# Performance work log

Measured on AMD Instinct MI355X. Metric: run time of the kernel, lower is better.

The kernel has to match this reference:

```python
import jax, jax.numpy as jnp
import numpy as np

B, S, D = 32, 4096, 256

def setup_inputs() -> dict:
    key = jax.random.key(0)
    k1, k2, k3 = jax.random.split(key, 3)
    inputs = jax.random.normal(k1, (B, S, D), dtype=jnp.float32)
    W = jax.random.normal(k2, (D, D), dtype=jnp.float32) * 0.05  # 'random_normal' init
    b = jnp.zeros((D,), dtype=jnp.float32)
    V = jax.random.normal(k3, (D, 1), dtype=jnp.float32) * 0.05
    return {"inputs": inputs, "W": W, "b": b, "V": V}

def reference(inputs, W, b, V):
    # score: [B,S,D] = tanh(inputs @ W + b)
    score = jnp.tanh(jnp.einsum('bsd,de->bse', inputs, W) + b)
    # logits: [B,S,1]; softmax over seq axis (axis=1)
    logits = jnp.einsum('bsd,do->bso', score, V)
    attn = jax.nn.softmax(logits, axis=1)            # [B,S,1]
    # weighted sum pooling over seq -> [B,D]
    context = jnp.sum(attn * inputs, axis=1)
    return context
```

## Files before the change

kernel.cpp:

```cpp
#include <hip/hip_runtime.h>
#include <hip/hip_bf16.h>

#define DD 256
#define SS 4096

typedef __bf16 bf16x8 __attribute__((ext_vector_type(8)));
typedef float  f32x4  __attribute__((ext_vector_type(4)));

__device__ __forceinline__ float fast_tanh(float x) {
  float e = __expf(2.0f * x);
  return 1.0f - 2.0f / (e + 1.0f);
}

template<int CTRL>
__device__ __forceinline__ float dpp_mov(float v) {
  return __int_as_float(__builtin_amdgcn_update_dpp(0, __float_as_int(v), CTRL, 0xF, 0xF, true));
}
__device__ __forceinline__ float row16_sum(float v) {
  v += dpp_mov<0xB1>(v);
  v += dpp_mov<0x4E>(v);
  v += dpp_mov<0x124>(v);
  v += dpp_mov<0x128>(v);
  return v;
}
__device__ __forceinline__ float row16_max(float v) {
  v = fmaxf(v, dpp_mov<0xB1>(v));
  v = fmaxf(v, dpp_mov<0x4E>(v));
  v = fmaxf(v, dpp_mov<0x124>(v));
  v = fmaxf(v, dpp_mov<0x128>(v));
  return v;
}

__global__ __launch_bounds__(1024, 1) __attribute__((amdgpu_waves_per_eu(4)))
void fused_kernel(
    const float* __restrict__ X, const float* __restrict__ W,
    const float* __restrict__ bias, const float* __restrict__ V,
    float* __restrict__ Pout, float* __restrict__ Mout, float* __restrict__ Sout)
{
  __shared__ __bf16 WtF[8192 * 8];
  __shared__ float  Pacc[16][DD];
  __shared__ float  Vs[DD];
  __shared__ float  Bs[DD];
  __shared__ float  wred[16];
  __shared__ float  sred[16];

  const int t = threadIdx.x;
  for (int c = t; c < 8192; c += 1024) {
    const int lane_c = c & 63;
    const int ks  = (c >> 6) & 7;
    const int n0  = c >> 9;
    const int col = n0 * 16 + (lane_c & 15);
    const int k0  = ks * 32 + (lane_c >> 4) * 8;
    const float* wp = W + k0 * DD + col;
    bf16x8 fr;
    #pragma unroll
    for (int i = 0; i < 8; ++i) fr[i] = (__bf16)wp[i * DD];
    *reinterpret_cast<bf16x8*>(&WtF[(size_t)c * 8]) = fr;
  }
  if (t < DD) { Vs[t] = V[t]; Bs[t] = bias[t]; }
  __syncthreads();

  const int wave = t >> 6, lane = t & 63;
  const int g  = lane >> 4;
  const int lg = lane & 15;
  const size_t rowBase = (size_t)blockIdx.x * 512 + (size_t)wave * 32;

  bf16x8 a[2][8];
  #pragma unroll
  for (int st = 0; st < 2; ++st) {
    const float* xr = X + (rowBase + st * 16 + lg) * DD;
    #pragma unroll
    for (int ks = 0; ks < 8; ++ks) {
      const float4* p = reinterpret_cast<const float4*>(xr + ks * 32 + g * 8);
      float4 f0 = p[0], f1 = p[1];
      bf16x8 fr;
      fr[0] = (__bf16)f0.x; fr[1] = (__bf16)f0.y; fr[2] = (__bf16)f0.z; fr[3] = (__bf16)f0.w;
      fr[4] = (__bf16)f1.x; fr[5] = (__bf16)f1.y; fr[6] = (__bf16)f1.z; fr[7] = (__bf16)f1.w;
      a[st][ks] = fr;
    }
  }

  float sp0[4] = {0.f,0.f,0.f,0.f};
  float sp1[4] = {0.f,0.f,0.f,0.f};
  #pragma unroll 1
  for (int n0 = 0; n0 < 16; ++n0) {
    const __bf16* bp = WtF + ((size_t)(n0 * 8) * 64 + lane) * 8;
    f32x4 acc0 = {0.f,0.f,0.f,0.f};
    f32x4 acc1 = {0.f,0.f,0.f,0.f};
    #pragma unroll
    for (int ks = 0; ks < 8; ++ks) {
      bf16x8 bfr = *reinterpret_cast<const bf16x8*>(bp + (size_t)ks * 64 * 8);
      acc0 = __builtin_amdgcn_mfma_f32_16x16x32_bf16(a[0][ks], bfr, acc0, 0, 0, 0);
      acc1 = __builtin_amdgcn_mfma_f32_16x16x32_bf16(a[1][ks], bfr, acc1, 0, 0, 0);
    }
    const int col = n0 * 16 + lg;
    const float vc = Vs[col], bc = Bs[col];
    #pragma unroll
    for (int r = 0; r < 4; ++r) {
      sp0[r] += fast_tanh(acc0[r] + bc) * vc;
      sp1[r] += fast_tanh(acc1[r] + bc) * vc;
    }
  }

  #pragma unroll
  for (int r = 0; r < 4; ++r) { sp0[r] = row16_sum(sp0[r]); sp1[r] = row16_sum(sp1[r]); }

  const int src = ((lg >> 2) << 4) | lg;
  float l0 = 0.f, l1 = 0.f;
  #pragma unroll
  for (int r = 0; r < 4; ++r) {
    float v0 = __shfl(sp0[r], src, 64);
    float v1 = __shfl(sp1[r], src, 64);
    if ((lg & 3) == r) { l0 = v0; l1 = v1; }
  }

  float wm = row16_max(fmaxf(l0, l1));
  if (lane == 0) wred[wave] = wm;
  __syncthreads();
  float M = -1e30f;
  #pragma unroll
  for (int w = 0; w < 16; ++w) M = fmaxf(M, wred[w]);

  const float w0 = __expf(l0 - M);
  const float w1 = __expf(l1 - M);

  float se = row16_sum(w0 + w1);
  if (lane == 0) sred[wave] = se;

  #pragma unroll
  for (int ks = 0; ks < 8; ++ks) {
    float p8[8];
    #pragma unroll
    for (int i = 0; i < 8; ++i)
      p8[i] = w0 * (float)a[0][ks][i] + w1 * (float)a[1][ks][i];
    #pragma unroll
    for (int i = 0; i < 8; ++i) p8[i] = row16_sum(p8[i]);
    if (lg < 2) {
      float4 v = (lg == 0) ? make_float4(p8[0], p8[1], p8[2], p8[3])
                           : make_float4(p8[4], p8[5], p8[6], p8[7]);
      *reinterpret_cast<float4*>(&Pacc[wave][ks * 32 + g * 8 + lg * 4]) = v;
    }
  }
  __syncthreads();

  if (t < DD) {
    float s = 0.f;
    #pragma unroll
    for (int w = 0; w < 16; ++w) s += Pacc[w][t];
    Pout[(size_t)blockIdx.x * DD + t] = s;
  }
  if (t == 0) {
    float ss = 0.f;
    #pragma unroll
    for (int w = 0; w < 16; ++w) ss += sred[w];
    Sout[blockIdx.x] = ss;
    Mout[blockIdx.x] = M;
  }
}

__global__ __launch_bounds__(256) void combine_kernel(
    const float* __restrict__ P, const float* __restrict__ Mb,
    const float* __restrict__ Sb, float* __restrict__ ctx)
{
  const int b = blockIdx.x, t = threadIdx.x;
  float Mg = -1e30f;
  #pragma unroll
  for (int k = 0; k < 8; ++k) Mg = fmaxf(Mg, Mb[b * 8 + k]);
  float denom = 0.f, acc = 0.f;
  #pragma unroll
  for (int k = 0; k < 8; ++k) {
    const float f = __expf(Mb[b * 8 + k] - Mg);
    denom += f * Sb[b * 8 + k];
    acc   += f * P[(size_t)(b * 8 + k) * DD + t];
  }
  ctx[b * DD + t] = acc / denom;
}

extern "C" void kernel_launch(void* const* d_in, const int* in_sizes, int n_in,
                              void* d_out, int out_size, void* d_ws, size_t ws_size,
                              hipStream_t stream) {
  const float* X    = (const float*)d_in[0];
  const float* W    = (const float*)d_in[1];
  const float* bias = (const float*)d_in[2];
  const float* V    = (const float*)d_in[3];
  float* ctx = (float*)d_out;

  float* P = (float*)d_ws;
  float* M = P + 256 * DD;
  float* S = M + 256;

  fused_kernel<<<256, 1024, 0, stream>>>(X, W, bias, V, P, M, S);
  combine_kernel<<<32, 256, 0, stream>>>(P, M, S, ctx);
}
```

Baseline: 51.45 us.

## Pre-swizzle W to bf16 in global memory and stream B-fragments with double buffering

W is now converted and swizzled to bf16 fragments once by a separate prep kernel into workspace, instead of every block rebuilding a 128KB LDS copy. The fused kernel reads B fragments straight from global/L2 with a two-buffer register prefetch, and uses 512 blocks of 512 threads, so more blocks fit per CU and more waves are resident. This removes the per-block W staging cost and the large LDS footprint, at the cost of an extra launch, repeated L2 reads of W, more register pressure, and a combine over 16 partials per batch.

```diff
diff --git a/kernel.cpp b/kernel.cpp
--- a/kernel.cpp
+++ b/kernel.cpp
@@ -31,39 +31,61 @@
   return v;
 }
 
-__global__ __launch_bounds__(1024, 1) __attribute__((amdgpu_waves_per_eu(4)))
-void fused_kernel(
-    const float* __restrict__ X, const float* __restrict__ W,
+__global__ __launch_bounds__(256) void prep_kernel(
+    const float* __restrict__ W, __bf16* __restrict__ WF)
+{
+  const int c = blockIdx.x * 256 + threadIdx.x;
+  const int lane_c = c & 63;
+  const int ks  = (c >> 6) & 7;
+  const int n0  = c >> 9;
+  const int col = n0 * 16 + (lane_c & 15);
+  const int k0  = ks * 32 + (lane_c >> 4) * 8;
+  const float* wp = W + k0 * DD + col;
+  bf16x8 fr;
+  #pragma unroll
+  for (int i = 0; i < 8; ++i) fr[i] = (__bf16)wp[i * DD];
+  *reinterpret_cast<bf16x8*>(WF + (size_t)c * 8) = fr;
+}
+
+#define LOADB(buf, n0q) { \
+  const bf16x8* _src = WFv + ((n0q) * 8 * 64 + lane); \
+  _Pragma("unroll") \
+  for (int _ks = 0; _ks < 8; ++_ks) buf[_ks] = _src[_ks * 64]; }
+
+#define COMPUTE(buf, n0q) { \
+  f32x4 _acc0 = {0.f,0.f,0.f,0.f}; \
+  f32x4 _acc1 = {0.f,0.f,0.f,0.f}; \
+  _Pragma("unroll") \
+  for (int _ks = 0; _ks < 8; ++_ks) { \
+    _acc0 = __builtin_amdgcn_mfma_f32_16x16x32_bf16(a[0][_ks], buf[_ks], _acc0, 0, 0, 0); \
+    _acc1 = __builtin_amdgcn_mfma_f32_16x16x32_bf16(a[1][_ks], buf[_ks], _acc1, 0, 0, 0); } \
+  const int _col = (n0q) * 16 + lg; \
+  const float _vc = Vs[_col], _bc = Bs[_col]; \
+  _Pragma("unroll") \
+  for (int _r = 0; _r < 4; ++_r) { \
+    sp0[_r] += fast_tanh(_acc0[_r] + _bc) * _vc; \
+    sp1[_r] += fast_tanh(_acc1[_r] + _bc) * _vc; } }
+
+__global__ __launch_bounds__(512, 4) void fused_kernel(
+    const float* __restrict__ X, const __bf16* __restrict__ WF,
     const float* __restrict__ bias, const float* __restrict__ V,
     float* __restrict__ Pout, float* __restrict__ Mout, float* __restrict__ Sout)
 {
-  __shared__ __bf16 WtF[8192 * 8];
-  __shared__ float  Pacc[16][DD];
-  __shared__ float  Vs[DD];
-  __shared__ float  Bs[DD];
-  __shared__ float  wred[16];
-  __shared__ float  sred[16];
+  __shared__ float Pacc[8][DD];
+  __shared__ float Vs[DD];
+  __shared__ float Bs[DD];
+  __shared__ float wred[8];
+  __shared__ float sred[8];
 
   const int t = threadIdx.x;
-  for (int c = t; c < 8192; c += 1024) {
-    const int lane_c = c & 63;
-    const int ks  = (c >> 6) & 7;
-    const int n0  = c >> 9;
-    const int col = n0 * 16 + (lane_c & 15);
-    const int k0  = ks * 32 + (lane_c >> 4) * 8;
-    const float* wp = W + k0 * DD + col;
-    bf16x8 fr;
-    #pragma unroll
-    for (int i = 0; i < 8; ++i) fr[i] = (__bf16)wp[i * DD];
-    *reinterpret_cast<bf16x8*>(&WtF[(size_t)c * 8]) = fr;
-  }
   if (t < DD) { Vs[t] = V[t]; Bs[t] = bias[t]; }
   __syncthreads();
 
   const int wave = t >> 6, lane = t & 63;
   const int g  = lane >> 4;
   const int lg = lane & 15;
-  const size_t rowBase = (size_t)blockIdx.x * 512 + (size_t)wave * 32;
+  const size_t rowBase = (size_t)blockIdx.x * 256 + (size_t)wave * 32;
+  const bf16x8* WFv = reinterpret_cast<const bf16x8*>(WF);
 
   bf16x8 a[2][8];
   #pragma unroll
@@ -82,24 +104,14 @@
 
   float sp0[4] = {0.f,0.f,0.f,0.f};
   float sp1[4] = {0.f,0.f,0.f,0.f};
-  #pragma unroll 1
-  for (int n0 = 0; n0 < 16; ++n0) {
-    const __bf16* bp = WtF + ((size_t)(n0 * 8) * 64 + lane) * 8;
-    f32x4 acc0 = {0.f,0.f,0.f,0.f};
-    f32x4 acc1 = {0.f,0.f,0.f,0.f};
-    #pragma unroll
-    for (int ks = 0; ks < 8; ++ks) {
-      bf16x8 bfr = *reinterpret_cast<const bf16x8*>(bp + (size_t)ks * 64 * 8);
-      acc0 = __builtin_amdgcn_mfma_f32_16x16x32_bf16(a[0][ks], bfr, acc0, 0, 0, 0);
-      acc1 = __builtin_amdgcn_mfma_f32_16x16x32_bf16(a[1][ks], bfr, acc1, 0, 0, 0);
-    }
-    const int col = n0 * 16 + lg;
-    const float vc = Vs[col], bc = Bs[col];
-    #pragma unroll
-    for (int r = 0; r < 4; ++r) {
-      sp0[r] += fast_tanh(acc0[r] + bc) * vc;
-      sp1[r] += fast_tanh(acc1[r] + bc) * vc;
-    }
+  bf16x8 bufA[8], bufB[8];
+  LOADB(bufA, 0);
+  #pragma unroll
+  for (int n2 = 0; n2 < 8; ++n2) {
+    LOADB(bufB, n2 * 2 + 1);
+    COMPUTE(bufA, n2 * 2);
+    if (n2 < 7) LOADB(bufA, n2 * 2 + 2);
+    COMPUTE(bufB, n2 * 2 + 1);
   }
 
   #pragma unroll
@@ -119,7 +131,7 @@
   __syncthreads();
   float M = -1e30f;
   #pragma unroll
-  for (int w = 0; w < 16; ++w) M = fmaxf(M, wred[w]);
+  for (int w = 0; w < 8; ++w) M = fmaxf(M, wred[w]);
 
   const float w0 = __expf(l0 - M);
   const float w1 = __expf(l1 - M);
@@ -146,13 +158,13 @@
   if (t < DD) {
     float s = 0.f;
     #pragma unroll
-    for (int w = 0; w < 16; ++w) s += Pacc[w][t];
+    for (int w = 0; w < 8; ++w) s += Pacc[w][t];
     Pout[(size_t)blockIdx.x * DD + t] = s;
   }
   if (t == 0) {
     float ss = 0.f;
     #pragma unroll
-    for (int w = 0; w < 16; ++w) ss += sred[w];
+    for (int w = 0; w < 8; ++w) ss += sred[w];
     Sout[blockIdx.x] = ss;
     Mout[blockIdx.x] = M;
   }
@@ -165,13 +177,13 @@
   const int b = blockIdx.x, t = threadIdx.x;
   float Mg = -1e30f;
   #pragma unroll
-  for (int k = 0; k < 8; ++k) Mg = fmaxf(Mg, Mb[b * 8 + k]);
+  for (int k = 0; k < 16; ++k) Mg = fmaxf(Mg, Mb[b * 16 + k]);
   float denom = 0.f, acc = 0.f;
   #pragma unroll
-  for (int k = 0; k < 8; ++k) {
-    const float f = __expf(Mb[b * 8 + k] - Mg);
-    denom += f * Sb[b * 8 + k];
-    acc   += f * P[(size_t)(b * 8 + k) * DD + t];
+  for (int k = 0; k < 16; ++k) {
+    const float f = __expf(Mb[b * 16 + k] - Mg);
+    denom += f * Sb[b * 16 + k];
+    acc   += f * P[(size_t)(b * 16 + k) * DD + t];
   }
   ctx[b * DD + t] = acc / denom;
 }
@@ -185,10 +197,12 @@
   const float* V    = (const float*)d_in[3];
   float* ctx = (float*)d_out;
 
-  float* P = (float*)d_ws;
-  float* M = P + 256 * DD;
-  float* S = M + 256;
-
-  fused_kernel<<<256, 1024, 0, stream>>>(X, W, bias, V, P, M, S);
+  __bf16* WF = (__bf16*)d_ws;
+  float* P = (float*)((char*)d_ws + 128 * 1024);
+  float* M = P + 512 * DD;
+  float* S = M + 512;
+
+  prep_kernel<<<32, 256, 0, stream>>>(W, WF);
+  fused_kernel<<<512, 512, 0, stream>>>(X, WF, bias, V, P, M, S);
   combine_kernel<<<32, 256, 0, stream>>>(P, M, S, ctx);
 }
```

After: 57.54 us. 1.12x slower.

## Pre-swizzle W in separate kernel and overlap X loads with MFMA tiles

Applied to the files above, without the earlier changes.

Moves the W transpose and bf16 conversion into a small prep kernel writing a pre-swizzled buffer, so each block only does a straight vectorized copy into LDS. X loads are staged in chunks: the first 16 rows load before the LDS copy, and the second 16 rows load in halves while the first sub-tile's MFMA loop runs, hiding global latency. Each block now makes two single-accumulator passes instead of one interleaved pass. Also swaps __expf for exp2f with a prescaled constant in tanh. This adds a third kernel launch and a workspace round trip for W, and the single-accumulator loops expose more MFMA dependency latency.

```diff
diff --git a/kernel.cpp b/kernel.cpp
--- a/kernel.cpp
+++ b/kernel.cpp
@@ -8,7 +8,7 @@
 typedef float  f32x4  __attribute__((ext_vector_type(4)));
 
 __device__ __forceinline__ float fast_tanh(float x) {
-  float e = __expf(2.0f * x);
+  float e = exp2f(x * 2.885390081777927f);
   return 1.0f - 2.0f / (e + 1.0f);
 }
 
@@ -31,9 +31,49 @@
   return v;
 }
 
+__global__ __launch_bounds__(256) void prep_kernel(
+    const float* __restrict__ W, __bf16* __restrict__ WF)
+{
+  const int c = blockIdx.x * 256 + threadIdx.x;
+  const int lane_c = c & 63;
+  const int ks  = (c >> 6) & 7;
+  const int n0  = c >> 9;
+  const int col = n0 * 16 + (lane_c & 15);
+  const int k0  = ks * 32 + (lane_c >> 4) * 8;
+  const float* wp = W + k0 * DD + col;
+  bf16x8 fr;
+  #pragma unroll
+  for (int i = 0; i < 8; ++i) fr[i] = (__bf16)wp[i * DD];
+  *reinterpret_cast<bf16x8*>(WF + (size_t)c * 8) = fr;
+}
+
+#define PACK(dst, f0, f1) { \
+  bf16x8 _fr; \
+  _fr[0] = (__bf16)(f0).x; _fr[1] = (__bf16)(f0).y; \
+  _fr[2] = (__bf16)(f0).z; _fr[3] = (__bf16)(f0).w; \
+  _fr[4] = (__bf16)(f1).x; _fr[5] = (__bf16)(f1).y; \
+  _fr[6] = (__bf16)(f1).z; _fr[7] = (__bf16)(f1).w; \
+  (dst) = _fr; }
+
+#define TILE(aX, spX, n0q) { \
+  const __bf16* _bp = WtF + ((size_t)((n0q) * 8 * 64 + lane)) * 8; \
+  bf16x8 _bfr[8]; \
+  _Pragma("unroll") \
+  for (int _ks = 0; _ks < 8; ++_ks) \
+    _bfr[_ks] = *reinterpret_cast<const bf16x8*>(_bp + (size_t)_ks * 512); \
+  f32x4 _acc = {0.f, 0.f, 0.f, 0.f}; \
+  _Pragma("unroll") \
+  for (int _ks = 0; _ks < 8; ++_ks) \
+    _acc = __builtin_amdgcn_mfma_f32_16x16x32_bf16(aX[_ks], _bfr[_ks], _acc, 0, 0, 0); \
+  const int _col = (n0q) * 16 + lg; \
+  const float _vc = Vs[_col], _bc = Bs[_col]; \
+  _Pragma("unroll") \
+  for (int _r = 0; _r < 4; ++_r) \
+    spX[_r] += fast_tanh(_acc[_r] + _bc) * _vc; }
+
 __global__ __launch_bounds__(1024, 1) __attribute__((amdgpu_waves_per_eu(4)))
 void fused_kernel(
-    const float* __restrict__ X, const float* __restrict__ W,
+    const float* __restrict__ X, const __bf16* __restrict__ WF,
     const float* __restrict__ bias, const float* __restrict__ V,
     float* __restrict__ Pout, float* __restrict__ Mout, float* __restrict__ Sout)
 {
@@ -45,62 +85,63 @@
   __shared__ float  sred[16];
 
   const int t = threadIdx.x;
-  for (int c = t; c < 8192; c += 1024) {
-    const int lane_c = c & 63;
-    const int ks  = (c >> 6) & 7;
-    const int n0  = c >> 9;
-    const int col = n0 * 16 + (lane_c & 15);
-    const int k0  = ks * 32 + (lane_c >> 4) * 8;
-    const float* wp = W + k0 * DD + col;
-    bf16x8 fr;
-    #pragma unroll
-    for (int i = 0; i < 8; ++i) fr[i] = (__bf16)wp[i * DD];
-    *reinterpret_cast<bf16x8*>(&WtF[(size_t)c * 8]) = fr;
-  }
-  if (t < DD) { Vs[t] = V[t]; Bs[t] = bias[t]; }
-  __syncthreads();
-
   const int wave = t >> 6, lane = t & 63;
   const int g  = lane >> 4;
   const int lg = lane & 15;
   const size_t rowBase = (size_t)blockIdx.x * 512 + (size_t)wave * 32;
 
-  bf16x8 a[2][8];
-  #pragma unroll
-  for (int st = 0; st < 2; ++st) {
-    const float* xr = X + (rowBase + st * 16 + lg) * DD;
-    #pragma unroll
-    for (int ks = 0; ks < 8; ++ks) {
-      const float4* p = reinterpret_cast<const float4*>(xr + ks * 32 + g * 8);
-      float4 f0 = p[0], f1 = p[1];
-      bf16x8 fr;
-      fr[0] = (__bf16)f0.x; fr[1] = (__bf16)f0.y; fr[2] = (__bf16)f0.z; fr[3] = (__bf16)f0.w;
-      fr[4] = (__bf16)f1.x; fr[5] = (__bf16)f1.y; fr[6] = (__bf16)f1.z; fr[7] = (__bf16)f1.w;
-      a[st][ks] = fr;
-    }
+  float4 raw[16];
+  const float* xr0 = X + (rowBase + lg) * DD;
+  #pragma unroll
+  for (int ks = 0; ks < 8; ++ks) {
+    const float4* p = reinterpret_cast<const float4*>(xr0 + ks * 32 + g * 8);
+    raw[2 * ks]     = p[0];
+    raw[2 * ks + 1] = p[1];
+  }
+
+  {
+    const uint4* src = reinterpret_cast<const uint4*>(WF);
+    uint4* dst = reinterpret_cast<uint4*>(WtF);
+    #pragma unroll
+    for (int i = 0; i < 8; ++i) dst[t + i * 1024] = src[t + i * 1024];
+  }
+  if (t < DD) { Vs[t] = V[t]; Bs[t] = bias[t]; }
+  __syncthreads();
+
+  bf16x8 a0[8], a1[8];
+  #pragma unroll
+  for (int ks = 0; ks < 8; ++ks) PACK(a0[ks], raw[2 * ks], raw[2 * ks + 1]);
+  const float* xr1 = X + (rowBase + 16 + lg) * DD;
+  #pragma unroll
+  for (int ks = 0; ks < 4; ++ks) {
+    const float4* p = reinterpret_cast<const float4*>(xr1 + ks * 32 + g * 8);
+    raw[2 * ks]     = p[0];
+    raw[2 * ks + 1] = p[1];
   }
 
   float sp0[4] = {0.f,0.f,0.f,0.f};
   float sp1[4] = {0.f,0.f,0.f,0.f};
+
   #pragma unroll 1
-  for (int n0 = 0; n0 < 16; ++n0) {
-    const __bf16* bp = WtF + ((size_t)(n0 * 8) * 64 + lane) * 8;
-    f32x4 acc0 = {0.f,0.f,0.f,0.f};
-    f32x4 acc1 = {0.f,0.f,0.f,0.f};
-    #pragma unroll
-    for (int ks = 0; ks < 8; ++ks) {
-      bf16x8 bfr = *reinterpret_cast<const bf16x8*>(bp + (size_t)ks * 64 * 8);
-      acc0 = __builtin_amdgcn_mfma_f32_16x16x32_bf16(a[0][ks], bfr, acc0, 0, 0, 0);
-      acc1 = __builtin_amdgcn_mfma_f32_16x16x32_bf16(a[1][ks], bfr, acc1, 0, 0, 0);
-    }
-    const int col = n0 * 16 + lg;
-    const float vc = Vs[col], bc = Bs[col];
-    #pragma unroll
-    for (int r = 0; r < 4; ++r) {
-      sp0[r] += fast_tanh(acc0[r] + bc) * vc;
-      sp1[r] += fast_tanh(acc1[r] + bc) * vc;
-    }
-  }
+  for (int n0 = 0; n0 < 8; ++n0) TILE(a0, sp0, n0);
+
+  #pragma unroll
+  for (int ks = 0; ks < 4; ++ks) PACK(a1[ks], raw[2 * ks], raw[2 * ks + 1]);
+  #pragma unroll
+  for (int ks = 4; ks < 8; ++ks) {
+    const float4* p = reinterpret_cast<const float4*>(xr1 + ks * 32 + g * 8);
+    raw[2 * (ks - 4)]     = p[0];
+    raw[2 * (ks - 4) + 1] = p[1];
+  }
+
+  #pragma unroll 1
+  for (int n0 = 8; n0 < 16; ++n0) TILE(a0, sp0, n0);
+
+  #pragma unroll
+  for (int ks = 4; ks < 8; ++ks) PACK(a1[ks], raw[2 * (ks - 4)], raw[2 * (ks - 4) + 1]);
+
+  #pragma unroll 1
+  for (int n0 = 0; n0 < 16; ++n0) TILE(a1, sp1, n0);
 
   #pragma unroll
   for (int r = 0; r < 4; ++r) { sp0[r] = row16_sum(sp0[r]); sp1[r] = row16_sum(sp1[r]); }
@@ -132,7 +173,7 @@
     float p8[8];
     #pragma unroll
     for (int i = 0; i < 8; ++i)
-      p8[i] = w0 * (float)a[0][ks][i] + w1 * (float)a[1][ks][i];
+      p8[i] = w0 * (float)a0[ks][i] + w1 * (float)a1[ks][i];
     #pragma unroll
     for (int i = 0; i < 8; ++i) p8[i] = row16_sum(p8[i]);
     if (lg < 2) {
@@ -185,10 +226,12 @@
   const float* V    = (const float*)d_in[3];
   float* ctx = (float*)d_out;
 
-  float* P = (float*)d_ws;
+  __bf16* WF = (__bf16*)d_ws;
+  float* P = (float*)((char*)d_ws + 128 * 1024);
   float* M = P + 256 * DD;
   float* S = M + 256;
 
-  fused_kernel<<<256, 1024, 0, stream>>>(X, W, bias, V, P, M, S);
+  prep_kernel<<<32, 256, 0, stream>>>(W, WF);
+  fused_kernel<<<256, 1024, 0, stream>>>(X, WF, bias, V, P, M, S);
   combine_kernel<<<32, 256, 0, stream>>>(P, M, S, ctx);
 }
```

Result: slower. 60.04 us (+16.7%).

## Pre-swizzle W to bf16 in separate kernel and overlap X loads with smem fill

Applied to the files above, without the earlier changes.

Adds a prep kernel that converts and swizzles W into bf16 MFMA fragment layout once, so each of the 256 fused blocks does a straight 128KB vector copy instead of strided fp32 gathers and per-element conversion. The barrier is moved after the X register loads so global X fetches overlap the shared-memory fill. The MFMA loop now preloads all B fragments, splits each accumulation into two independent chains to shorten dependency latency, and is unrolled by two. tanh uses exp2f with a folded constant. The extra kernel launch adds fixed overhead and more register pressure.

```diff
diff --git a/kernel.cpp b/kernel.cpp
--- a/kernel.cpp
+++ b/kernel.cpp
@@ -8,7 +8,7 @@
 typedef float  f32x4  __attribute__((ext_vector_type(4)));
 
 __device__ __forceinline__ float fast_tanh(float x) {
-  float e = __expf(2.0f * x);
+  float e = exp2f(x * 2.885390081777927f);
   return 1.0f - 2.0f / (e + 1.0f);
 }
 
@@ -31,9 +31,25 @@
   return v;
 }
 
+__global__ __launch_bounds__(256) void prep_kernel(
+    const float* __restrict__ W, __bf16* __restrict__ WF)
+{
+  const int c = blockIdx.x * 256 + threadIdx.x;
+  const int lane_c = c & 63;
+  const int ks  = (c >> 6) & 7;
+  const int n0  = c >> 9;
+  const int col = n0 * 16 + (lane_c & 15);
+  const int k0  = ks * 32 + (lane_c >> 4) * 8;
+  const float* wp = W + k0 * DD + col;
+  bf16x8 fr;
+  #pragma unroll
+  for (int i = 0; i < 8; ++i) fr[i] = (__bf16)wp[i * DD];
+  *reinterpret_cast<bf16x8*>(WF + (size_t)c * 8) = fr;
+}
+
 __global__ __launch_bounds__(1024, 1) __attribute__((amdgpu_waves_per_eu(4)))
 void fused_kernel(
-    const float* __restrict__ X, const float* __restrict__ W,
+    const float* __restrict__ X, const __bf16* __restrict__ WF,
     const float* __restrict__ bias, const float* __restrict__ V,
     float* __restrict__ Pout, float* __restrict__ Mout, float* __restrict__ Sout)
 {
@@ -45,30 +61,22 @@
   __shared__ float  sred[16];
 
   const int t = threadIdx.x;
-  for (int c = t; c < 8192; c += 1024) {
-    const int lane_c = c & 63;
-    const int ks  = (c >> 6) & 7;
-    const int n0  = c >> 9;
-    const int col = n0 * 16 + (lane_c & 15);
-    const int k0  = ks * 32 + (lane_c >> 4) * 8;
-    const float* wp = W + k0 * DD + col;
-    bf16x8 fr;
-    #pragma unroll
-    for (int i = 0; i < 8; ++i) fr[i] = (__bf16)wp[i * DD];
-    *reinterpret_cast<bf16x8*>(&WtF[(size_t)c * 8]) = fr;
-  }
-  if (t < DD) { Vs[t] = V[t]; Bs[t] = bias[t]; }
-  __syncthreads();
-
   const int wave = t >> 6, lane = t & 63;
   const int g  = lane >> 4;
   const int lg = lane & 15;
   const size_t rowBase = (size_t)blockIdx.x * 512 + (size_t)wave * 32;
 
-  bf16x8 a[2][8];
-  #pragma unroll
-  for (int st = 0; st < 2; ++st) {
-    const float* xr = X + (rowBase + st * 16 + lg) * DD;
+  {
+    const uint4* src = reinterpret_cast<const uint4*>(WF);
+    uint4* dst = reinterpret_cast<uint4*>(WtF);
+    #pragma unroll
+    for (int i = 0; i < 8; ++i) dst[t + i * 1024] = src[t + i * 1024];
+  }
+  if (t < DD) { Vs[t] = V[t]; Bs[t] = bias[t]; }
+
+  bf16x8 a0[8], a1[8];
+  {
+    const float* xr = X + (rowBase + lg) * DD;
     #pragma unroll
     for (int ks = 0; ks < 8; ++ks) {
       const float4* p = reinterpret_cast<const float4*>(xr + ks * 32 + g * 8);
@@ -76,29 +84,47 @@
       bf16x8 fr;
       fr[0] = (__bf16)f0.x; fr[1] = (__bf16)f0.y; fr[2] = (__bf16)f0.z; fr[3] = (__bf16)f0.w;
       fr[4] = (__bf16)f1.x; fr[5] = (__bf16)f1.y; fr[6] = (__bf16)f1.z; fr[7] = (__bf16)f1.w;
-      a[st][ks] = fr;
-    }
-  }
+      a0[ks] = fr;
+    }
+  }
+  {
+    const float* xr = X + (rowBase + 16 + lg) * DD;
+    #pragma unroll
+    for (int ks = 0; ks < 8; ++ks) {
+      const float4* p = reinterpret_cast<const float4*>(xr + ks * 32 + g * 8);
+      float4 f0 = p[0], f1 = p[1];
+      bf16x8 fr;
+      fr[0] = (__bf16)f0.x; fr[1] = (__bf16)f0.y; fr[2] = (__bf16)f0.z; fr[3] = (__bf16)f0.w;
+      fr[4] = (__bf16)f1.x; fr[5] = (__bf16)f1.y; fr[6] = (__bf16)f1.z; fr[7] = (__bf16)f1.w;
+      a1[ks] = fr;
+    }
+  }
+  __syncthreads();
 
   float sp0[4] = {0.f,0.f,0.f,0.f};
   float sp1[4] = {0.f,0.f,0.f,0.f};
-  #pragma unroll 1
+  #pragma unroll 2
   for (int n0 = 0; n0 < 16; ++n0) {
-    const __bf16* bp = WtF + ((size_t)(n0 * 8) * 64 + lane) * 8;
-    f32x4 acc0 = {0.f,0.f,0.f,0.f};
-    f32x4 acc1 = {0.f,0.f,0.f,0.f};
-    #pragma unroll
-    for (int ks = 0; ks < 8; ++ks) {
-      bf16x8 bfr = *reinterpret_cast<const bf16x8*>(bp + (size_t)ks * 64 * 8);
-      acc0 = __builtin_amdgcn_mfma_f32_16x16x32_bf16(a[0][ks], bfr, acc0, 0, 0, 0);
-      acc1 = __builtin_amdgcn_mfma_f32_16x16x32_bf16(a[1][ks], bfr, acc1, 0, 0, 0);
+    const __bf16* bp = WtF + ((size_t)(n0 * 8 * 64 + lane)) * 8;
+    bf16x8 bfr[8];
+    #pragma unroll
+    for (int ks = 0; ks < 8; ++ks)
+      bfr[ks] = *reinterpret_cast<const bf16x8*>(bp + (size_t)ks * 512);
+    f32x4 p0 = {0.f,0.f,0.f,0.f}, p1 = {0.f,0.f,0.f,0.f};
+    f32x4 q0 = {0.f,0.f,0.f,0.f}, q1 = {0.f,0.f,0.f,0.f};
+    #pragma unroll
+    for (int ks = 0; ks < 4; ++ks) {
+      p0 = __builtin_amdgcn_mfma_f32_16x16x32_bf16(a0[ks],     bfr[ks],     p0, 0, 0, 0);
+      q0 = __builtin_amdgcn_mfma_f32_16x16x32_bf16(a1[ks],     bfr[ks],     q0, 0, 0, 0);
+      p1 = __builtin_amdgcn_mfma_f32_16x16x32_bf16(a0[ks + 4], bfr[ks + 4], p1, 0, 0, 0);
+      q1 = __builtin_amdgcn_mfma_f32_16x16x32_bf16(a1[ks + 4], bfr[ks + 4], q1, 0, 0, 0);
     }
     const int col = n0 * 16 + lg;
     const float vc = Vs[col], bc = Bs[col];
     #pragma unroll
     for (int r = 0; r < 4; ++r) {
-      sp0[r] += fast_tanh(acc0[r] + bc) * vc;
-      sp1[r] += fast_tanh(acc1[r] + bc) * vc;
+      sp0[r] += fast_tanh((p0[r] + p1[r]) + bc) * vc;
+      sp1[r] += fast_tanh((q0[r] + q1[r]) + bc) * vc;
     }
   }
 
@@ -132,7 +158,7 @@
     float p8[8];
     #pragma unroll
     for (int i = 0; i < 8; ++i)
-      p8[i] = w0 * (float)a[0][ks][i] + w1 * (float)a[1][ks][i];
+      p8[i] = w0 * (float)a0[ks][i] + w1 * (float)a1[ks][i];
     #pragma unroll
     for (int i = 0; i < 8; ++i) p8[i] = row16_sum(p8[i]);
     if (lg < 2) {
@@ -185,10 +211,12 @@
   const float* V    = (const float*)d_in[3];
   float* ctx = (float*)d_out;
 
-  float* P = (float*)d_ws;
+  __bf16* WF = (__bf16*)d_ws;
+  float* P = (float*)((char*)d_ws + 128 * 1024);
   float* M = P + 256 * DD;
   float* S = M + 256;
 
-  fused_kernel<<<256, 1024, 0, stream>>>(X, W, bias, V, P, M, S);
+  prep_kernel<<<32, 256, 0, stream>>>(W, WF);
+  fused_kernel<<<256, 1024, 0, stream>>>(X, WF, bias, V, P, M, S);
   combine_kernel<<<32, 256, 0, stream>>>(P, M, S, ctx);
 }
```

Measured after the change: 66.77 us. +29.8%, slower.
